# Kernel optimization log

Measured on AMD Instinct MI355X. Metric: run time of the kernel, lower is better.

## Reference

```python
import jax, jax.numpy as jnp
import numpy as np

B, S, E = 2, 2048, 1024
H = 1344            # hidden_dim = ceil(1.3*1024/64)*64
NH = 4              # mLSTM heads
DH = H // NH        # 336
K = 4               # causal conv kernel size
NPH = H // 4        # headwise proj heads (qkv_proj_blocksize=4)
PD = H // NPH       # per-head proj dim = 4
EPS = 1e-6


def setup_inputs() -> dict:
    key = jax.random.key(0)
    ks = jax.random.split(key, 10)
    s_in = jnp.sqrt(2.0 / (5 * E))    # small_init(E)
    s_pd = jnp.sqrt(2.0 / (5 * PD))   # small_init per-head dim
    return {
        "x": jax.random.normal(ks[0], (B, S, E), jnp.float32),
        "W_up": jax.random.normal(ks[1], (E, 2 * H), jnp.float32) * s_in,
        "conv_k": jax.random.normal(ks[2], (K, 1, H), jnp.float32) * jnp.sqrt(2.0 / K),  # depthwise, WIO layout
        "conv_b": jnp.zeros((H,), jnp.float32),
        "Wq": jax.random.normal(ks[3], (NPH, PD, PD), jnp.float32) * s_pd,
        "Wk": jax.random.normal(ks[4], (NPH, PD, PD), jnp.float32) * s_pd,
        "Wv": jax.random.normal(ks[5], (NPH, PD, PD), jnp.float32) * s_pd,
        "W_ig": jax.random.normal(ks[6], (3 * H, NH), jnp.float32) * 0.01,
        "b_ig": jax.random.normal(ks[7], (NH,), jnp.float32) * 0.1,
        "W_fg": jax.random.normal(ks[8], (3 * H, NH), jnp.float32) * 0.01,
        "b_fg": jnp.linspace(3.0, 6.0, NH, dtype=jnp.float32),
        "ln_w": jnp.ones((H,), jnp.float32),
        "skip": jnp.ones((H,), jnp.float32),
        "W_down": jax.random.normal(ks[9], (H, E), jnp.float32) * (2.0 / 12 / np.sqrt(H)),
    }


def _headwise(x, W):
    # LinearHeadwiseExpand: block-diagonal projection over NPH heads of size PD
    xh = x.reshape(B, S, NPH, PD)
    return jnp.einsum('bshd,hdo->bsho', xh, W).reshape(B, S, H)


def _mlstm_cell(q, k, v, ig, fg):
    # parallel stabilized mLSTM; q,k,v: (B,NH,S,DH); ig,fg: (B,NH,S)
    logf = jax.nn.log_sigmoid(fg)
    c = jnp.cumsum(logf, axis=-1)                         # (B,NH,S)
    logfmat = c[..., :, None] - c[..., None, :]           # (B,NH,S,S) cumulative forget decay
    mask = jnp.tril(jnp.ones((S, S), bool))               # causal mask
    log_D = jnp.where(mask, logfmat, -jnp.inf) + ig[..., None, :]
    m = jnp.max(log_D, axis=-1, keepdims=True)            # rowwise stabilizer
    D = jnp.exp(log_D - m)
    qk = jnp.einsum('bnsd,bntd->bnst', q, k) * (DH ** -0.5)
    C = qk * D
    n = jnp.maximum(jnp.abs(jnp.sum(C, axis=-1, keepdims=True)), jnp.exp(-m))
    return jnp.einsum('bnst,bntd->bnsd', C / (n + EPS), v)


def reference(x, W_up, conv_k, conv_b, Wq, Wk, Wv, W_ig, b_ig, W_fg, b_fg, ln_w, skip, W_down):
    x_inner = x @ W_up                                    # (B,S,2H)
    x_m, z = jnp.split(x_inner, 2, axis=-1)
    # depthwise causal conv1d
    xp = jnp.pad(x_m, ((0, 0), (K - 1, 0), (0, 0)))
    xc = jax.lax.conv_general_dilated(
        xp, conv_k, (1,), 'VALID',
        dimension_numbers=('NWC', 'WIO', 'NWC'),
        feature_group_count=H) + conv_b
    act = jax.nn.silu(xc)
    q = _headwise(act, Wq)
    k = _headwise(act, Wk)
    v = _headwise(x_m, Wv)
    gin = jnp.concatenate([q, k, v], axis=-1)             # (B,S,3H)
    ig = jnp.transpose(gin @ W_ig + b_ig, (0, 2, 1))      # (B,NH,S)
    fg = jnp.transpose(gin @ W_fg + b_fg, (0, 2, 1))
    qh = jnp.transpose(q.reshape(B, S, NH, DH), (0, 2, 1, 3))
    kh = jnp.transpose(k.reshape(B, S, NH, DH), (0, 2, 1, 3))
    vh = jnp.transpose(v.reshape(B, S, NH, DH), (0, 2, 1, 3))
    h = _mlstm_cell(qh, kh, vh, ig, fg)                   # (B,NH,S,DH)
    # multi-head layernorm (per-head groupnorm over DH, scale only)
    mu = jnp.mean(h, axis=-1, keepdims=True)
    var = jnp.var(h, axis=-1, keepdims=True)
    hn = (h - mu) * jax.lax.rsqrt(var + 1e-5) * ln_w.reshape(NH, 1, DH)
    h_out = jnp.transpose(hn, (0, 2, 1, 3)).reshape(B, S, H)
    h_state = (h_out + skip * act) * jax.nn.silu(z)
    return h_state @ W_down
```

## Files before the change

### kernel.cpp

```cpp
#include <hip/hip_runtime.h>
#include <cmath>

#define DI __device__ __forceinline__

constexpr int B_=2, S_=2048, E_=1024, H_=1344, NH_=4, DH_=336;
constexpr int BS_=B_*S_, H2_=2*H_;
constexpr int NG_=B_*NH_*S_;

constexpr size_t N_X=(size_t)BS_*E_;
constexpr size_t N_WUP=(size_t)E_*H2_;
constexpr size_t N_WDN=(size_t)H_*E_;
constexpr size_t N_BSH=(size_t)BS_*H_;
constexpr size_t N_BSH2=(size_t)BS_*H2_;
constexpr size_t N_WH=5376, N_WG=16128, N_CK=4*H_;

constexpr size_t O_IGB = 64;
constexpr size_t O_LOGF= O_IGB + NG_;
constexpr size_t O_AB  = O_LOGF+ NG_;
constexpr size_t O_MB  = O_AB  + NG_;
constexpr size_t O_MTB = O_MB  + NG_;
constexpr size_t O_CK  = O_MTB + NG_;
constexpr size_t O_CB  = O_CK  + N_CK;
constexpr size_t O_WQ  = O_CB  + H_;
constexpr size_t O_WK  = O_WQ  + N_WH;
constexpr size_t O_WV  = O_WK  + N_WH;
constexpr size_t O_WIG = O_WV  + N_WH;
constexpr size_t O_BIG = O_WIG + N_WG;
constexpr size_t O_WFG = O_BIG + 16;
constexpr size_t O_BFG = O_WFG + N_WG;
constexpr size_t O_LNW = O_BFG + 16;
constexpr size_t O_SKP = O_LNW + H_;
constexpr size_t O_FX  = O_SKP + H_;
constexpr size_t O_FWUP= O_FX  + N_X;
constexpr size_t O_FWDN= O_FWUP+ N_WUP;
constexpr size_t O_XIN = O_FWDN+ N_WDN;
constexpr size_t O_ACT = O_XIN + N_BSH2;
constexpr size_t O_QB  = O_ACT + N_BSH;
constexpr size_t O_KB  = O_QB  + N_BSH;
constexpr size_t O_VB  = O_KB  + N_BSH;
constexpr size_t O_HOUT= O_VB  + N_BSH;

constexpr size_t KSPLIT_SHORTS=(size_t)8*128*11*64*8;
constexpr size_t VT_SHORTS=(size_t)8*64*22*64*8;

typedef __attribute__((ext_vector_type(8))) short bf16x8;
typedef __attribute__((ext_vector_type(4))) float f32x4;

DI float bf2f(unsigned int u){union{unsigned int i;float f;}v;v.i=(u&0xffffu)<<16;return v.f;}
DI unsigned short f2bf(float f){union{float f;unsigned int i;}v;v.f=f;unsigned int x=v.i;
  return (unsigned short)((x+0x7fffu+((x>>16)&1u))>>16);}
DI float siluf(float x){return x/(1.f+expf(-x));}
DI float logsigf(float x){return (x>=0.f)?-log1pf(expf(-x)):x-log1pf(expf(x));}
DI void load4(const float* p, float* d){float4 v=*reinterpret_cast<const float4*>(p);
  d[0]=v.x;d[1]=v.y;d[2]=v.z;d[3]=v.w;}

__global__ __launch_bounds__(256) void detect_k(const unsigned short* __restrict__ xraw,
                                                int* __restrict__ flag){
  __shared__ int cnt_s;
  if(threadIdx.x==0) cnt_s=0;
  __syncthreads();
  int c=0;
  for(int i=threadIdx.x;i<2048;i+=256){
    const unsigned e=(xraw[i]>>7)&0xFFu;
    if(e>=0x90u) c++;
  }
  atomicAdd(&cnt_s,c);
  __syncthreads();
  if(threadIdx.x==0) *flag=(cnt_s>16)?0:1;
}

constexpr int CV0=5376, CV1=CV0+1344, CV2=CV1+5376, CV3=CV2+5376, CV4=CV3+5376,
              CV5=CV4+16128, CV6=CV5+4, CV7=CV6+16128, CV8=CV7+4,
              CV9=CV8+1344, CVT=CV9+1344;
__global__ __launch_bounds__(256) void convall_k(
    const void* s0,const void* s1,const void* s2,const void* s3,const void* s4,
    const void* s5,const void* s6,const void* s7,const void* s8,const void* s9,
    const void* s10, float* __restrict__ ws, const int* __restrict__ flag){
  const int i=blockIdx.x*256+threadIdx.x;
  if(i>=CVT) return;
  const void* src; int off; size_t dst;
  if(i<CV0){src=s0; off=i;      dst=O_CK +off;}
  else if(i<CV1){src=s1; off=i-CV0; dst=O_CB +off;}
  else if(i<CV2){src=s2; off=i-CV1; dst=O_WQ +off;}
  else if(i<CV3){src=s3; off=i-CV2; dst=O_WK +off;}
  else if(i<CV4){src=s4; off=i-CV3; dst=O_WV +off;}
  else if(i<CV5){src=s5; off=i-CV4; dst=O_WIG+off;}
  else if(i<CV6){src=s6; off=i-CV5; dst=O_BIG+off;}
  else if(i<CV7){src=s7; off=i-CV6; dst=O_WFG+off;}
  else if(i<CV8){src=s8; off=i-CV7; dst=O_BFG+off;}
  else if(i<CV9){src=s9; off=i-CV8; dst=O_LNW+off;}
  else          {src=s10;off=i-CV9; dst=O_SKP+off;}
  ws[dst]=(*flag)?bf2f(((const unsigned short*)src)[off])
                 :((const float*)src)[off];
}

__global__ __launch_bounds__(256) void prepAB_k(const void* __restrict__ xsrc,
    const void* __restrict__ wsrc, const int* __restrict__ flag,
    unsigned short* __restrict__ xhi, unsigned short* __restrict__ xlo,
    unsigned short* __restrict__ whi, unsigned short* __restrict__ wlo){
  const int blk=blockIdx.x;
  const int fl=*flag;
  float v[8];
  unsigned short* dh; unsigned short* dl; size_t slot;
  if(blk<2048){
    slot=(size_t)blk*256+threadIdx.x;
    const int l=(int)slot&63, rest=(int)(slot>>6);
    const int kc=rest&31, mt=rest>>5;
    const int row=mt*16+(l&15), k0=kc*32+(l>>4)*8;
    if(fl){
      const unsigned short* s=(const unsigned short*)xsrc+(size_t)row*1024+k0;
      const uint4 u=*reinterpret_cast<const uint4*>(s);
      v[0]=bf2f(u.x);v[1]=bf2f(u.x>>16);v[2]=bf2f(u.y);v[3]=bf2f(u.y>>16);
      v[4]=bf2f(u.z);v[5]=bf2f(u.z>>16);v[6]=bf2f(u.w);v[7]=bf2f(u.w>>16);
    }else{
      const float* s=(const float*)xsrc+(size_t)row*1024+k0;
      load4(s,v); load4(s+4,v+4);
    }
    dh=xhi; dl=xlo;
  } else {
    slot=(size_t)(blk-2048)*256+threadIdx.x;
    const int l=(int)slot&63, rest=(int)(slot>>6);
    const int kc=rest&31, nt=rest>>5;
    const int col=nt*16+(l&15), row0=kc*32+(l>>4)*8;
    if(fl){
      const unsigned short* s=(const unsigned short*)wsrc;
#pragma unroll
      for(int j=0;j<8;j++) v[j]=bf2f(s[(size_t)(row0+j)*2688+col]);
    }else{
      const float* s=(const float*)wsrc;
#pragma unroll
      for(int j=0;j<8;j++) v[j]=s[(size_t)(row0+j)*2688+col];
    }
    dh=whi; dl=wlo;
  }
  unsigned short h8[8], l8[8];
#pragma unroll
  for(int j=0;j<8;j++){ h8[j]=f2bf(v[j]); l8[j]=f2bf(v[j]-bf2f(h8[j])); }
  uint4 ph,pl;
  ph.x=(unsigned)h8[0]|((unsigned)h8[1]<<16); ph.y=(unsigned)h8[2]|((unsigned)h8[3]<<16);
  ph.z=(unsigned)h8[4]|((unsigned)h8[5]<<16); ph.w=(unsigned)h8[6]|((unsigned)h8[7]<<16);
  pl.x=(unsigned)l8[0]|((unsigned)l8[1]<<16); pl.y=(unsigned)l8[2]|((unsigned)l8[3]<<16);
  pl.z=(unsigned)l8[4]|((unsigned)l8[5]<<16); pl.w=(unsigned)l8[6]|((unsigned)l8[7]<<16);
  *reinterpret_cast<uint4*>(&dh[slot*8])=ph;
  *reinterpret_cast<uint4*>(&dl[slot*8])=pl;
}

__global__ __launch_bounds__(256) void gemm3_k(
    const unsigned short* __restrict__ Ahi, const unsigned short* __restrict__ Alo,
    const unsigned short* __restrict__ Bhi, const unsigned short* __restrict__ Blo,
    void* __restrict__ C, const int* __restrict__ flag, int kcn, int ldc){
  const int t=threadIdx.x, w=t>>6, l=t&63, lm=l&15, quad=l>>4;
  const int bn=blockIdx.x*128, bm=blockIdx.y*128;
  const int mtg0=bm>>4, ntg0=bn>>4;

  __shared__ short TT[2][32*512];

  f32x4 acc[2][8];
#pragma unroll
  for(int g=0;g<2;g++)
#pragma unroll
    for(int nt=0;nt<8;nt++) acc[g][nt]={0.f,0.f,0.f,0.f};

  auto stage=[&](int buf,int kc){
#pragma unroll
    for(int j=0;j<8;j++){
      const int tr=w*8+j;
      const unsigned short* src;
      if(tr<8)       src=&Ahi[((size_t)(mtg0+tr   )*kcn+kc)*512+(size_t)l*8];
      else if(tr<16) src=&Alo[((size_t)(mtg0+tr-8 )*kcn+kc)*512+(size_t)l*8];
      else if(tr<24) src=&Bhi[((size_t)(ntg0+tr-16)*kcn+kc)*512+(size_t)l*8];
      else           src=&Blo[((size_t)(ntg0+tr-24)*kcn+kc)*512+(size_t)l*8];
      __builtin_amdgcn_global_load_lds(
        (const __attribute__((address_space(1))) unsigned int*)src,
        (__attribute__((address_space(3))) unsigned int*)&TT[buf][tr*512],
        16,0,0);
    }
  };

  auto compute=[&](int buf){
    const short* Tb=&TT[buf][0];
    const bf16x8 ah0=*reinterpret_cast<const bf16x8*>(&Tb[(2*w  )*512+l*8]);
    const bf16x8 ah1=*reinterpret_cast<const bf16x8*>(&Tb[(2*w+1)*512+l*8]);
    const bf16x8 al0=*reinterpret_cast<const bf16x8*>(&Tb[(8+2*w  )*512+l*8]);
    const bf16x8 al1=*reinterpret_cast<const bf16x8*>(&Tb[(8+2*w+1)*512+l*8]);
#pragma unroll
    for(int nt=0;nt<8;nt++){
      const bf16x8 bh=*reinterpret_cast<const bf16x8*>(&Tb[(16+nt)*512+l*8]);
      const bf16x8 bl=*reinterpret_cast<const bf16x8*>(&Tb[(24+nt)*512+l*8]);
      acc[0][nt]=__builtin_amdgcn_mfma_f32_16x16x32_bf16(ah0,bh,acc[0][nt],0,0,0);
      acc[0][nt]=__builtin_amdgcn_mfma_f32_16x16x32_bf16(al0,bh,acc[0][nt],0,0,0);
      acc[0][nt]=__builtin_amdgcn_mfma_f32_16x16x32_bf16(ah0,bl,acc[0][nt],0,0,0);
      acc[1][nt]=__builtin_amdgcn_mfma_f32_16x16x32_bf16(ah1,bh,acc[1][nt],0,0,0);
      acc[1][nt]=__builtin_amdgcn_mfma_f32_16x16x32_bf16(al1,bh,acc[1][nt],0,0,0);
      acc[1][nt]=__builtin_amdgcn_mfma_f32_16x16x32_bf16(ah1,bl,acc[1][nt],0,0,0);
    }
  };

  stage(0,0);
  for(int kc=0;kc<kcn;kc++){
    const int cur=kc&1;
    if(kc+1<kcn){
      stage(cur^1,kc+1);
      asm volatile("s_waitcnt vmcnt(8)" ::: "memory");
    } else {
      asm volatile("s_waitcnt vmcnt(0)" ::: "memory");
    }
    __builtin_amdgcn_s_barrier();
    compute(cur);
    __builtin_amdgcn_s_barrier();
  }

  const int bf=flag?*flag:0;
#pragma unroll
  for(int g=0;g<2;g++)
#pragma unroll
    for(int nt=0;nt<8;nt++)
#pragma unroll
      for(int r=0;r<4;r++){
        const size_t idx=(size_t)(bm+(2*w+g)*16+quad*4+r)*ldc+bn+nt*16+lm;
        if(bf) ((unsigned short*)C)[idx]=f2bf(acc[g][nt][r]);
        else   ((float*)C)[idx]=acc[g][nt][r];
      }
}

__global__ __launch_bounds__(384) void convqkvgates_k(
    const float* __restrict__ xin, const float* __restrict__ ck,
    const float* __restrict__ cb,
    const float* __restrict__ Wq, const float* __restrict__ Wk,
    const float* __restrict__ Wv,
    const float* __restrict__ Wig, const float* __restrict__ big,
    const float* __restrict__ Wfg, const float* __restrict__ bfg,
    float* __restrict__ act, float* __restrict__ qb, float* __restrict__ kb,
    float* __restrict__ vb, float* __restrict__ igb, float* __restrict__ logfb){
  const int bs=blockIdx.x;
  const int b=bs>>11, s=bs&2047;
  const int t=threadIdx.x;
  __shared__ float4 sq4[336], sk4[336], sv4[336];
  __shared__ float red[6][8];
  if(t<336){
    const int ph=t, base=ph*4;
    float xc[4];
#pragma unroll
    for(int d=0;d<4;d++) xc[d]=cb[base+d];
    float xm[4]={0.f,0.f,0.f,0.f};
#pragma unroll
    for(int w=0;w<4;w++){
      const int sr=s-3+w;
      if(sr>=0){
        float xv[4];
        load4(&xin[(size_t)(b*S_+sr)*H2_+base],xv);
#pragma unroll
        for(int d=0;d<4;d++) xc[d]+=xv[d]*ck[w*H_+base+d];
        if(w==3){ xm[0]=xv[0];xm[1]=xv[1];xm[2]=xv[2];xm[3]=xv[3]; }
      }
    }
    float a4[4];
#pragma unroll
    for(int d=0;d<4;d++) a4[d]=siluf(xc[d]);
    *reinterpret_cast<float4*>(&act[(size_t)bs*H_+base])
        =make_float4(a4[0],a4[1],a4[2],a4[3]);
    float q4[4],k4[4],v4[4];
#pragma unroll
    for(int o=0;o<4;o++){
      float q=0.f,k=0.f,v=0.f;
#pragma unroll
      for(int d=0;d<4;d++){
        q+=a4[d]*Wq[ph*16+d*4+o];
        k+=a4[d]*Wk[ph*16+d*4+o];
        v+=xm[d]*Wv[ph*16+d*4+o];
      }
      q4[o]=q;k4[o]=k;v4[o]=v;
    }
    const int nh=ph/84, dh0=(ph-nh*84)*4;
    const size_t off=((size_t)(b*NH_+nh)*S_+s)*DH_+dh0;
    *reinterpret_cast<float4*>(&qb[off])=make_float4(q4[0],q4[1],q4[2],q4[3]);
    *reinterpret_cast<float4*>(&kb[off])=make_float4(k4[0],k4[1],k4[2],k4[3]);
    *reinterpret_cast<float4*>(&vb[off])=make_float4(v4[0],v4[1],v4[2],v4[3]);
    sq4[ph]=make_float4(q4[0],q4[1],q4[2],q4[3]);
    sk4[ph]=make_float4(k4[0],k4[1],k4[2],k4[3]);
    sv4[ph]=make_float4(v4[0],v4[1],v4[2],v4[3]);
  }
  __syncthreads();
  const float* sq=reinterpret_cast<const float*>(sq4);
  const float* sk=reinterpret_cast<const float*>(sk4);
  const float* sv=reinterpret_cast<const float*>(sv4);
  float aI0=0.f,aI1=0.f,aI2=0.f,aI3=0.f;
  float aF0=0.f,aF1=0.f,aF2=0.f,aF3=0.f;
  for(int h=t; h<H_; h+=384){
    const float q=sq[h], k=sk[h], v=sv[h];
    const float4 wiq=*reinterpret_cast<const float4*>(&Wig[(size_t)h*4]);
    const float4 wik=*reinterpret_cast<const float4*>(&Wig[(size_t)(H_+h)*4]);
    const float4 wiv=*reinterpret_cast<const float4*>(&Wig[(size_t)(2*H_+h)*4]);
    const float4 wfq=*reinterpret_cast<const float4*>(&Wfg[(size_t)h*4]);
    const float4 wfk=*reinterpret_cast<const float4*>(&Wfg[(size_t)(H_+h)*4]);
    const float4 wfv=*reinterpret_cast<const float4*>(&Wfg[(size_t)(2*H_+h)*4]);
    aI0+=q*wiq.x+k*wik.x+v*wiv.x;
    aI1+=q*wiq.y+k*wik.y+v*wiv.y;
    aI2+=q*wiq.z+k*wik.z+v*wiv.z;
    aI3+=q*wiq.w+k*wik.w+v*wiv.w;
    aF0+=q*wfq.x+k*wfk.x+v*wfv.x;
    aF1+=q*wfq.y+k*wfk.y+v*wfv.y;
    aF2+=q*wfq.z+k*wfk.z+v*wfv.z;
    aF3+=q*wfq.w+k*wfk.w+v*wfv.w;
  }
#pragma unroll
  for(int m=1;m<64;m<<=1){
    aI0+=__shfl_xor(aI0,m); aI1+=__shfl_xor(aI1,m);
    aI2+=__shfl_xor(aI2,m); aI3+=__shfl_xor(aI3,m);
    aF0+=__shfl_xor(aF0,m); aF1+=__shfl_xor(aF1,m);
    aF2+=__shfl_xor(aF2,m); aF3+=__shfl_xor(aF3,m);
  }
  const int wv=t>>6, l=t&63;
  if(l==0){
    red[wv][0]=aI0; red[wv][1]=aI1; red[wv][2]=aI2; red[wv][3]=aI3;
    red[wv][4]=aF0; red[wv][5]=aF1; red[wv][6]=aF2; red[wv][7]=aF3;
  }
  __syncthreads();
  if(t==0){
    float r[8];
#pragma unroll
    for(int j=0;j<8;j++){
      float a=0.f;
#pragma unroll
      for(int wv2=0;wv2<6;wv2++) a+=red[wv2][j];
      r[j]=a;
    }
#pragma unroll
    for(int n=0;n<4;n++){
      const size_t o=(size_t)(b*NH_+n)*S_+s;
      igb[o]=r[n]+big[n];
      logfb[o]=logsigf(r[4+n]+bfg[n]);
    }
  }
}

__global__ __launch_bounds__(256) void kvprep3_k(const float* __restrict__ kb,
                                                 const float* vb,
                                                 const void* __restrict__ wdnsrc,
                                                 const int* __restrict__ flag,
                                                 unsigned short* __restrict__ khi,
                                                 unsigned short* __restrict__ klo,
                                                 unsigned short* __restrict__ vTf,
                                                 unsigned short* __restrict__ wdnhi,
                                                 unsigned short* __restrict__ wdnlo,
                                                 float* partz){
  const int blk=blockIdx.x;
  if(blk<1024){
    const int head=blk>>7, tt=blk&127;
    const size_t obase=(size_t)blk*11*512;
    for(int slot=threadIdx.x; slot<704; slot+=256){
      const int dc=slot>>6, ll=slot&63, quad=ll>>4, lm=ll&15;
      const int tg=tt*16+lm, dbase=dc*32+quad*8;
      float v[8];
      if(dbase<336){
        load4(&kb[((size_t)head*S_+tg)*DH_+dbase],v);
        load4(&kb[((size_t)head*S_+tg)*DH_+dbase+4],v+4);
      } else { for(int j=0;j<8;j++) v[j]=0.f; }
      unsigned short hi8[8], lo8[8];
#pragma unroll
      for(int j=0;j<8;j++){
        hi8[j]=f2bf(v[j]);
        lo8[j]=f2bf(v[j]-bf2f(hi8[j]));
      }
      const size_t o=obase+(size_t)(dc*64+ll)*8;
      uint4 ph, pl;
      ph.x=(unsigned)hi8[0]|((unsigned)hi8[1]<<16); ph.y=(unsigned)hi8[2]|((unsigned)hi8[3]<<16);
      ph.z=(unsigned)hi8[4]|((unsigned)hi8[5]<<16); ph.w=(unsigned)hi8[6]|((unsigned)hi8[7]<<16);
      pl.x=(unsigned)lo8[0]|((unsigned)lo8[1]<<16); pl.y=(unsigned)lo8[2]|((unsigned)lo8[3]<<16);
      pl.z=(unsigned)lo8[4]|((unsigned)lo8[5]<<16); pl.w=(unsigned)lo8[6]|((unsigned)lo8[7]<<16);
      *reinterpret_cast<uint4*>(&khi[o])=ph;
      *reinterpret_cast<uint4*>(&klo[o])=pl;
    }
  } else if(blk<1536){
    const int vblk=blk-1024;
    const int head=vblk>>6, tc=vblk&63;
    const size_t obase=(size_t)vblk*22*512;
    for(int slot=threadIdx.x; slot<1408; slot+=256){
      const int ntg=slot>>6, ll=slot&63, quad=ll>>4, lm=ll&15;
      const int n=ntg*16+lm, t0=tc*32+quad*8;
      unsigned short h8[8];
#pragma unroll
      for(int j=0;j<8;j++){
        float val;
        if(n<336)       val=vb[((size_t)head*S_+t0+j)*DH_+n];
        else if(n==336) val=1.f;
        else            val=0.f;
        h8[j]=f2bf(val);
      }
      uint4 pk;
      pk.x=(unsigned)h8[0]|((unsigned)h8[1]<<16); pk.y=(unsigned)h8[2]|((unsigned)h8[3]<<16);
      pk.z=(unsigned)h8[4]|((unsigned)h8[5]<<16); pk.w=(unsigned)h8[6]|((unsigned)h8[7]<<16);
      *reinterpret_cast<uint4*>(&vTf[obase+(size_t)(ntg*64+ll)*8])=pk;
    }
    __syncthreads();
    const size_t zb=((size_t)head*2048+(size_t)tc*32)*336;
    for(int idx=threadIdx.x; idx<32*336; idx+=256) partz[zb+idx]=0.f;
  } else {
    const size_t slot=(size_t)(blk-1536)*256+threadIdx.x;
    const int l=(int)slot&63, rest=(int)(slot>>6);
    const int kc=rest%42, nt=rest/42;
    const int col=nt*16+(l&15), row0=kc*32+(l>>4)*8;
    const int fl=*flag;
    float v[8];
    if(fl){
      const unsigned short* s=(const unsigned short*)wdnsrc;
#pragma unroll
      for(int j=0;j<8;j++) v[j]=bf2f(s[(size_t)(row0+j)*1024+col]);
    }else{
      const float* s=(const float*)wdnsrc;
#pragma unroll
      for(int j=0;j<8;j++) v[j]=s[(size_t)(row0+j)*1024+col];
    }
    unsigned short h8[8], l8[8];
#pragma unroll
    for(int j=0;j<8;j++){ h8[j]=f2bf(v[j]); l8[j]=f2bf(v[j]-bf2f(h8[j])); }
    uint4 ph,pl;
    ph.x=(unsigned)h8[0]|((unsigned)h8[1]<<16); ph.y=(unsigned)h8[2]|((unsigned)h8[3]<<16);
    ph.z=(unsigned)h8[4]|((unsigned)h8[5]<<16); ph.w=(unsigned)h8[6]|((unsigned)h8[7]<<16);
    pl.x=(unsigned)l8[0]|((unsigned)l8[1]<<16); pl.y=(unsigned)l8[2]|((unsigned)l8[3]<<16);
    pl.z=(unsigned)l8[4]|((unsigned)l8[5]<<16); pl.w=(unsigned)l8[6]|((unsigned)l8[7]<<16);
    *reinterpret_cast<uint4*>(&wdnhi[slot*8])=ph;
    *reinterpret_cast<uint4*>(&wdnlo[slot*8])=pl;
  }
}

__global__ __launch_bounds__(256) void scan_k(float* igm,
                                              const float* __restrict__ logfb,
                                              float* __restrict__ ab,float* __restrict__ Mb,
                                              float* __restrict__ mtb){
  const int head=blockIdx.x, t=threadIdx.x;
  __shared__ float sh[256];
  const float* lf=logfb+(size_t)head*S_;
  float* ig=igm+(size_t)head*S_;
  float lc[8];
  float run=0.f;
#pragma unroll
  for(int i=0;i<8;i++){ run+=lf[t*8+i]; lc[i]=run; }
  sh[t]=run;
  for(int st=1;st<256;st<<=1){
    __syncthreads();
    const float v=(t>=st)?sh[t-st]:0.f;
    __syncthreads();
    sh[t]+=v;
  }
  __syncthreads();
  const float off=(t==0)?0.f:sh[t-1];
  __syncthreads();
  float av[8],mv[8],cv[8];
  float mrun=-1e30f;
#pragma unroll
  for(int i=0;i<8;i++){
    cv[i]=off+lc[i];
    av[i]=ig[t*8+i]-cv[i];
    mrun=fmaxf(mrun,av[i]);
    mv[i]=mrun;
  }
  sh[t]=mrun;
  for(int st=1;st<256;st<<=1){
    __syncthreads();
    const float v=(t>=st)?sh[t-st]:-1e30f;
    __syncthreads();
    sh[t]=fmaxf(sh[t],v);
  }
  __syncthreads();
  const float moff=(t==0)?-1e30f:sh[t-1];
#pragma unroll
  for(int i=0;i<8;i++){
    const float Mi=fmaxf(moff,mv[i]);
    const size_t j=(size_t)head*S_+t*8+i;
    ab[j]=av[i]; Mb[j]=Mi; mtb[j]=cv[i]+Mi;
    ig[t*8+i]=0.f;
  }
}

__global__ __launch_bounds__(512,1) void mlstm6_k(
    const float* __restrict__ qb, const unsigned short* __restrict__ khi,
    const unsigned short* __restrict__ klo, const unsigned short* __restrict__ vTf,
    const float* __restrict__ ab, const float* __restrict__ Mb,
    float* __restrict__ part, float* __restrict__ rsum){
  const int bid=blockIdx.x;
  const int head=bid&7;
  const int rest=bid>>3;
  const int pairI=rest&7, seg=rest>>3;
  const int t=threadIdx.x, w=t>>6, l=t&63, lm=l&15, quad=l>>4;

  __shared__ short KV[2][66*512];
  __shared__ short Sc[8][16][40];

  const size_t hb=(size_t)head*S_;
  const float scale=0.05455447256f;

  const int sbA=pairI, sbB=15-pairI;
  const int nA=pairI+1, nTot=17;

  bf16x8 qh[11], ql[11];
  f32x4 accO[22];
  float Mr[4];
  int ws0=sbA*128+w*16;

  auto loadQ=[&](int ws0_){
    const float* qrow=qb+(hb+ws0_+lm)*DH_;
#pragma unroll
    for(int dc=0;dc<11;dc++){
      const int dbase=dc*32+quad*8;
      float v[8];
      if(dbase<336){ load4(qrow+dbase,v); load4(qrow+dbase+4,v+4); }
      else { for(int j=0;j<8;j++) v[j]=0.f; }
#pragma unroll
      for(int j=0;j<8;j++){
        const unsigned short h=f2bf(v[j]);
        qh[dc][j]=(short)h;
        ql[dc][j]=(short)f2bf(v[j]-bf2f(h));
      }
    }
#pragma unroll
    for(int r=0;r<4;r++) Mr[r]=Mb[hb+ws0_+quad*4+r];
#pragma unroll
    for(int n=0;n<22;n++) accO[n]={0.f,0.f,0.f,0.f};
  };

  auto itemC=[&](int i)->int{
    return (i<nA)? (seg+4*i) : (seg+4*(i-nA));
  };

  auto stage=[&](int buf,int c){
    const size_t kbase=(((size_t)head*128+(size_t)(2*c))*11)*512+(size_t)l*8;
    const size_t vbase=(((size_t)head*64+(size_t)c)*22)*512+(size_t)l*8;
#pragma unroll
    for(int j=0;j<9;j++){
      const int tr=w+8*j;
      if(tr<66){
        const unsigned short* src;
        if(tr<22)      src=&khi[kbase+(size_t)tr*512];
        else if(tr<44) src=&klo[kbase+(size_t)(tr-22)*512];
        else           src=&vTf[vbase+(size_t)(tr-44)*512];
        __builtin_amdgcn_global_load_lds(
          (const __attribute__((address_space(1))) unsigned int*)src,
          (__attribute__((address_space(3))) unsigned int*)&KV[buf][(size_t)tr*512],
          16,0,0);
      }
    }
  };

  auto compute=[&](int c,int buf){
    const int t0=c<<5;
    if(t0>ws0+15) return;
    const float al0=ab[hb+t0+lm];
    const float al1=ab[hb+t0+16+lm];
#pragma unroll
    for(int tt=0;tt<2;tt++){
      f32x4 a0={0,0,0,0}, a1={0,0,0,0}, a2={0,0,0,0};
#pragma unroll
      for(int dc=0;dc<11;dc++){
        const bf16x8 kh=*reinterpret_cast<const bf16x8*>(&KV[buf][(tt*11+dc)*512+l*8]);
        const bf16x8 kl=*reinterpret_cast<const bf16x8*>(&KV[buf][(22+tt*11+dc)*512+l*8]);
        a0=__builtin_amdgcn_mfma_f32_16x16x32_bf16(qh[dc],kh,a0,0,0,0);
        a1=__builtin_amdgcn_mfma_f32_16x16x32_bf16(ql[dc],kh,a1,0,0,0);
        a2=__builtin_amdgcn_mfma_f32_16x16x32_bf16(qh[dc],kl,a2,0,0,0);
      }
      const float al=(tt==0)?al0:al1;
      const int tg=t0+tt*16+lm;
#pragma unroll
      for(int r=0;r<4;r++){
        const int srow=quad*4+r;
        const float qk=a0[r]+a1[r]+a2[r];
        const float e=fminf(al-Mr[r],0.f);
        const float msk=(tg<=ws0+srow)?1.f:0.f;
        Sc[w][srow][tt*16+lm]=(short)f2bf(msk*(qk*scale*expf(e)));
      }
    }
    const bf16x8 scf=*reinterpret_cast<const bf16x8*>(&Sc[w][lm][quad*8]);
#pragma unroll
    for(int nt=0;nt<22;nt++){
      const bf16x8 vf=*reinterpret_cast<const bf16x8*>(&KV[buf][(44+nt)*512+l*8]);
      accO[nt]=__builtin_amdgcn_mfma_f32_16x16x32_bf16(scf,vf,accO[nt],0,0,0);
    }
  };

  auto epilogue=[&](){
    const size_t pbase=(size_t)head*2048+ws0;
#pragma unroll
    for(int nt=0;nt<22;nt++){
      const int col=nt*16+lm;
#pragma unroll
      for(int r=0;r<4;r++){
        const int srow=quad*4+r;
        const float val=accO[nt][r];
        if(col<336){ if(val!=0.f) atomicAdd(&part[(pbase+srow)*336+col],val); }
        else if(col==336){ if(val!=0.f) atomicAdd(&rsum[pbase+srow],val); }
      }
    }
  };

  loadQ(ws0);
  stage(0,itemC(0));
  __syncthreads();
  int cur=0;
  for(int i=0;i<nTot;i++){
    if(i+1<nTot) stage(cur^1,itemC(i+1));
    compute(itemC(i),cur);
    if(i==nA-1){
      epilogue();
      ws0=sbB*128+w*16;
      loadQ(ws0);
    }
    __syncthreads();
    cur^=1;
  }
  epilogue();
}

__global__ __launch_bounds__(256) void finalize3_k(const float* __restrict__ part,
                                                   const float* __restrict__ rsum,
                                                   const float* __restrict__ mtb,
                                                   const float* __restrict__ lnw,
                                                   const float* __restrict__ skip,
                                                   const float* __restrict__ act,
                                                   const float* __restrict__ xin,
                                                   unsigned short* __restrict__ hshi,
                                                   unsigned short* __restrict__ hslo){
  const int sblk=blockIdx.x, head=blockIdx.y;
  const int bI=head>>2, nh=head&3;
  const int s0=sblk*32;
  const int t=threadIdx.x, row=t>>3, sub=t&7;
  __shared__ float red1[32][8], red2[32][8];
  __shared__ float mu_s[32], rs_s[32], inv_s[32];
  const size_t pbase=(size_t)head*2048+s0;
  const float* prow=part+(pbase+row)*336;
  float s1=0.f,s2=0.f;
  for(int c=sub;c<336;c+=8){ const float v=prow[c]; s1+=v; s2+=v*v; }
  red1[row][sub]=s1; red2[row][sub]=s2;
  __syncthreads();
  if(sub==0){
    float a1=0.f,a2=0.f;
#pragma unroll
    for(int j=0;j<8;j++){ a1+=red1[row][j]; a2+=red2[row][j]; }
    const float mt=mtb[(size_t)head*S_+s0+row];
    const float nn=fmaxf(fabsf(rsum[pbase+row]), expf(fminf(fmaxf(-mt,-60.f),60.f)));
    const float inv=1.f/(nn+1e-6f);
    const float mu=a1*inv/336.f;
    const float var=a2*inv*inv/336.f-mu*mu;
    inv_s[row]=inv; mu_s[row]=mu;
    rs_s[row]=rsqrtf(fmaxf(var,0.f)+1e-5f);
  }
  __syncthreads();
  const float inv=inv_s[row], mu=mu_s[row], rs=rs_s[row];
  const size_t gbs=(size_t)(bI*S_+s0+row);
  const float* arow=act+gbs*H_+nh*DH_;
  const float* zrow=xin+gbs*H2_+H_+nh*DH_;
  const float* srw=skip+nh*DH_;
  const float* lrw=lnw+nh*DH_;
  const size_t mtbase=(gbs>>4)*42;
  const int lbase=(int)(gbs&15);
  for(int c=sub;c<336;c+=8){
    const float hn=(prow[c]*inv-mu)*rs*lrw[c];
    const float val=(hn+srw[c]*arow[c])*siluf(zrow[c]);
    const int h=nh*DH_+c;
    const int kc=h>>5, quad=(h>>3)&3, j=h&7;
    const size_t slot=(mtbase+kc)*64+lbase+16*quad;
    const unsigned short hi=f2bf(val);
    hshi[slot*8+j]=hi;
    hslo[slot*8+j]=f2bf(val-bf2f(hi));
  }
}

extern "C" void kernel_launch(void* const* d_in, const int* in_sizes, int n_in,
                              void* d_out, int out_size, void* d_ws, size_t ws_size,
                              hipStream_t stream){
  float* ws=(float*)d_ws;
  int* flag=(int*)ws;

  float* igb  = ws+O_IGB;
  float* logfb= ws+O_LOGF;
  float* ab   = ws+O_AB;
  float* Mbuf = ws+O_MB;
  float* mtb  = ws+O_MTB;
  float* f_ck = ws+O_CK;
  float* f_cb = ws+O_CB;
  float* f_wq = ws+O_WQ;
  float* f_wk = ws+O_WK;
  float* f_wv = ws+O_WV;
  float* f_wig= ws+O_WIG;
  float* f_big= ws+O_BIG;
  float* f_wfg= ws+O_WFG;
  float* f_bfg= ws+O_BFG;
  float* f_lnw= ws+O_LNW;
  float* f_skp= ws+O_SKP;
  float* xin  = ws+O_XIN;
  float* act  = ws+O_ACT;
  float* qb   = ws+O_QB;
  float* kb   = ws+O_KB;
  float* vb   = ws+O_VB;

  unsigned short* xhi  =(unsigned short*)(ws+O_FX);   unsigned short* xlo  =xhi+N_X;
  unsigned short* wuphi=(unsigned short*)(ws+O_FWUP); unsigned short* wuplo=wuphi+N_WUP;
  unsigned short* wdnhi=(unsigned short*)(ws+O_FWDN); unsigned short* wdnlo=wdnhi+N_WDN;
  unsigned short* khi=(unsigned short*)(ws+O_FX);
  unsigned short* klo=khi+KSPLIT_SHORTS;
  unsigned short* vTf=(unsigned short*)(ws+O_HOUT);
  unsigned short* hshi=(unsigned short*)kb;
  unsigned short* hslo=hshi+N_BSH;
  float* partb=vb;
  float* rsumb=igb;

  detect_k<<<1,256,0,stream>>>((const unsigned short*)d_in[0],flag);
  convall_k<<<(CVT+255)/256,256,0,stream>>>(d_in[2],d_in[3],d_in[4],d_in[5],d_in[6],
                                            d_in[7],d_in[8],d_in[9],d_in[10],d_in[11],
                                            d_in[12],ws,flag);

  prepAB_k<<<2048+1344,256,0,stream>>>(d_in[0],d_in[1],flag,xhi,xlo,wuphi,wuplo);
  gemm3_k<<<dim3(2688/128,4096/128),256,0,stream>>>(xhi,xlo,wuphi,wuplo,xin,nullptr,32,H2_);

  convqkvgates_k<<<BS_,384,0,stream>>>(xin,f_ck,f_cb,f_wq,f_wk,f_wv,
                                       f_wig,f_big,f_wfg,f_bfg,
                                       act,qb,kb,vb,igb,logfb);
  kvprep3_k<<<1024+512+672,256,0,stream>>>(kb,vb,d_in[13],flag,
                                           khi,klo,vTf,wdnhi,wdnlo,partb);
  scan_k<<<B_*NH_,256,0,stream>>>(igb,logfb,ab,Mbuf,mtb);
  mlstm6_k<<<256,512,0,stream>>>(qb,khi,klo,vTf,ab,Mbuf,partb,rsumb);
  finalize3_k<<<dim3(S_/32,B_*NH_),256,0,stream>>>(partb,rsumb,mtb,f_lnw,f_skp,act,xin,
                                                   hshi,hslo);
  gemm3_k<<<dim3(1024/128,4096/128),256,0,stream>>>(hshi,hslo,wdnhi,wdnlo,d_out,flag,42,E_);
}
```

Before: 438.5 us.

## Fuse K hi/lo split into gate kernel and parameter conversion into prepAB

The K tensor's bf16 hi/lo split and MFMA-tiled layout are now written directly from the conv/qkv/gates kernel, so the fp32 K buffer is no longer stored and re-read by a separate prep kernel. The small parameter conversion kernel is folded into prepAB as extra blocks, which removes one launch. The padding region of the K tiles is zeroed by extra blocks in the renamed V/W prep kernel. In exchange, the gate kernel's stores become scattered 8-byte writes.

New measurement: 431.0 us. About the same (-1.7%).

```diff
diff --git a/kernel.cpp b/kernel.cpp
--- a/kernel.cpp
+++ b/kernel.cpp
@@ -72,34 +72,35 @@
 constexpr int CV0=5376, CV1=CV0+1344, CV2=CV1+5376, CV3=CV2+5376, CV4=CV3+5376,
               CV5=CV4+16128, CV6=CV5+4, CV7=CV6+16128, CV8=CV7+4,
               CV9=CV8+1344, CVT=CV9+1344;
-__global__ __launch_bounds__(256) void convall_k(
-    const void* s0,const void* s1,const void* s2,const void* s3,const void* s4,
-    const void* s5,const void* s6,const void* s7,const void* s8,const void* s9,
-    const void* s10, float* __restrict__ ws, const int* __restrict__ flag){
-  const int i=blockIdx.x*256+threadIdx.x;
-  if(i>=CVT) return;
-  const void* src; int off; size_t dst;
-  if(i<CV0){src=s0; off=i;      dst=O_CK +off;}
-  else if(i<CV1){src=s1; off=i-CV0; dst=O_CB +off;}
-  else if(i<CV2){src=s2; off=i-CV1; dst=O_WQ +off;}
-  else if(i<CV3){src=s3; off=i-CV2; dst=O_WK +off;}
-  else if(i<CV4){src=s4; off=i-CV3; dst=O_WV +off;}
-  else if(i<CV5){src=s5; off=i-CV4; dst=O_WIG+off;}
-  else if(i<CV6){src=s6; off=i-CV5; dst=O_BIG+off;}
-  else if(i<CV7){src=s7; off=i-CV6; dst=O_WFG+off;}
-  else if(i<CV8){src=s8; off=i-CV7; dst=O_BFG+off;}
-  else if(i<CV9){src=s9; off=i-CV8; dst=O_LNW+off;}
-  else          {src=s10;off=i-CV9; dst=O_SKP+off;}
-  ws[dst]=(*flag)?bf2f(((const unsigned short*)src)[off])
-                 :((const float*)src)[off];
-}
 
 __global__ __launch_bounds__(256) void prepAB_k(const void* __restrict__ xsrc,
     const void* __restrict__ wsrc, const int* __restrict__ flag,
     unsigned short* __restrict__ xhi, unsigned short* __restrict__ xlo,
-    unsigned short* __restrict__ whi, unsigned short* __restrict__ wlo){
+    unsigned short* __restrict__ whi, unsigned short* __restrict__ wlo,
+    const void* s2,const void* s3,const void* s4,const void* s5,const void* s6,
+    const void* s7,const void* s8,const void* s9,const void* s10,const void* s11,
+    const void* s12, float* __restrict__ ws){
   const int blk=blockIdx.x;
   const int fl=*flag;
+  if(blk>=3392){
+    const int i=(blk-3392)*256+threadIdx.x;
+    if(i>=CVT) return;
+    const void* src; int off; size_t dst;
+    if(i<CV0){src=s2; off=i;      dst=O_CK +off;}
+    else if(i<CV1){src=s3; off=i-CV0; dst=O_CB +off;}
+    else if(i<CV2){src=s4; off=i-CV1; dst=O_WQ +off;}
+    else if(i<CV3){src=s5; off=i-CV2; dst=O_WK +off;}
+    else if(i<CV4){src=s6; off=i-CV3; dst=O_WV +off;}
+    else if(i<CV5){src=s7; off=i-CV4; dst=O_WIG+off;}
+    else if(i<CV6){src=s8; off=i-CV5; dst=O_BIG+off;}
+    else if(i<CV7){src=s9; off=i-CV6; dst=O_WFG+off;}
+    else if(i<CV8){src=s10;off=i-CV7; dst=O_BFG+off;}
+    else if(i<CV9){src=s11;off=i-CV8; dst=O_LNW+off;}
+    else          {src=s12;off=i-CV9; dst=O_SKP+off;}
+    ws[dst]=fl?bf2f(((const unsigned short*)src)[off])
+              :((const float*)src)[off];
+    return;
+  }
   float v[8];
   unsigned short* dh; unsigned short* dl; size_t slot;
   if(blk<2048){
@@ -230,8 +231,9 @@
     const float* __restrict__ Wv,
     const float* __restrict__ Wig, const float* __restrict__ big,
     const float* __restrict__ Wfg, const float* __restrict__ bfg,
-    float* __restrict__ act, float* __restrict__ qb, float* __restrict__ kb,
-    float* __restrict__ vb, float* __restrict__ igb, float* __restrict__ logfb){
+    float* __restrict__ act, float* __restrict__ qb, float* __restrict__ vb,
+    unsigned short* __restrict__ khi, unsigned short* __restrict__ klo,
+    float* __restrict__ igb, float* __restrict__ logfb){
   const int bs=blockIdx.x;
   const int b=bs>>11, s=bs&2047;
   const int t=threadIdx.x;
@@ -274,8 +276,27 @@
     const int nh=ph/84, dh0=(ph-nh*84)*4;
     const size_t off=((size_t)(b*NH_+nh)*S_+s)*DH_+dh0;
     *reinterpret_cast<float4*>(&qb[off])=make_float4(q4[0],q4[1],q4[2],q4[3]);
-    *reinterpret_cast<float4*>(&kb[off])=make_float4(k4[0],k4[1],k4[2],k4[3]);
     *reinterpret_cast<float4*>(&vb[off])=make_float4(v4[0],v4[1],v4[2],v4[3]);
+    {
+      const int head8=b*NH_+nh;
+      const int tt=s>>4, lm=s&15;
+      const int dc=dh0>>5, quad=(dh0&31)>>3, j=dh0&7;
+      const size_t ob=(((size_t)(head8*128+tt)*11)+dc)*512
+                      +(size_t)(quad*16+lm)*8+j;
+      unsigned short kh[4], kl[4];
+#pragma unroll
+      for(int o=0;o<4;o++){
+        kh[o]=f2bf(k4[o]);
+        kl[o]=f2bf(k4[o]-bf2f(kh[o]));
+      }
+      uint2 pk, pl;
+      pk.x=(unsigned)kh[0]|((unsigned)kh[1]<<16);
+      pk.y=(unsigned)kh[2]|((unsigned)kh[3]<<16);
+      pl.x=(unsigned)kl[0]|((unsigned)kl[1]<<16);
+      pl.y=(unsigned)kl[2]|((unsigned)kl[3]<<16);
+      *reinterpret_cast<uint2*>(&khi[ob])=pk;
+      *reinterpret_cast<uint2*>(&klo[ob])=pl;
+    }
     sq4[ph]=make_float4(q4[0],q4[1],q4[2],q4[3]);
     sk4[ph]=make_float4(k4[0],k4[1],k4[2],k4[3]);
     sv4[ph]=make_float4(v4[0],v4[1],v4[2],v4[3]);
@@ -334,47 +355,19 @@
   }
 }
 
-__global__ __launch_bounds__(256) void kvprep3_k(const float* __restrict__ kb,
-                                                 const float* vb,
-                                                 const void* __restrict__ wdnsrc,
-                                                 const int* __restrict__ flag,
-                                                 unsigned short* __restrict__ khi,
-                                                 unsigned short* __restrict__ klo,
-                                                 unsigned short* __restrict__ vTf,
-                                                 unsigned short* __restrict__ wdnhi,
-                                                 unsigned short* __restrict__ wdnlo,
-                                                 float* partz){
+__global__ __launch_bounds__(256) void vwprep_k(const float* vb,
+                                                const void* __restrict__ wdnsrc,
+                                                const int* __restrict__ flag,
+                                                unsigned short* __restrict__ vTf,
+                                                unsigned short* __restrict__ wdnhi,
+                                                unsigned short* __restrict__ wdnlo,
+                                                unsigned short* __restrict__ khi,
+                                                unsigned short* __restrict__ klo,
+                                                float* partz){
   const int blk=blockIdx.x;
-  if(blk<1024){
-    const int head=blk>>7, tt=blk&127;
-    const size_t obase=(size_t)blk*11*512;
-    for(int slot=threadIdx.x; slot<704; slot+=256){
-      const int dc=slot>>6, ll=slot&63, quad=ll>>4, lm=ll&15;
-      const int tg=tt*16+lm, dbase=dc*32+quad*8;
-      float v[8];
-      if(dbase<336){
-        load4(&kb[((size_t)head*S_+tg)*DH_+dbase],v);
-        load4(&kb[((size_t)head*S_+tg)*DH_+dbase+4],v+4);
-      } else { for(int j=0;j<8;j++) v[j]=0.f; }
-      unsigned short hi8[8], lo8[8];
-#pragma unroll
-      for(int j=0;j<8;j++){
-        hi8[j]=f2bf(v[j]);
-        lo8[j]=f2bf(v[j]-bf2f(hi8[j]));
-      }
-      const size_t o=obase+(size_t)(dc*64+ll)*8;
-      uint4 ph, pl;
-      ph.x=(unsigned)hi8[0]|((unsigned)hi8[1]<<16); ph.y=(unsigned)hi8[2]|((unsigned)hi8[3]<<16);
-      ph.z=(unsigned)hi8[4]|((unsigned)hi8[5]<<16); ph.w=(unsigned)hi8[6]|((unsigned)hi8[7]<<16);
-      pl.x=(unsigned)lo8[0]|((unsigned)lo8[1]<<16); pl.y=(unsigned)lo8[2]|((unsigned)lo8[3]<<16);
-      pl.z=(unsigned)lo8[4]|((unsigned)lo8[5]<<16); pl.w=(unsigned)lo8[6]|((unsigned)lo8[7]<<16);
-      *reinterpret_cast<uint4*>(&khi[o])=ph;
-      *reinterpret_cast<uint4*>(&klo[o])=pl;
-    }
-  } else if(blk<1536){
-    const int vblk=blk-1024;
-    const int head=vblk>>6, tc=vblk&63;
-    const size_t obase=(size_t)vblk*22*512;
+  if(blk<512){
+    const int head=blk>>6, tc=blk&63;
+    const size_t obase=(size_t)blk*22*512;
     for(int slot=threadIdx.x; slot<1408; slot+=256){
       const int ntg=slot>>6, ll=slot&63, quad=ll>>4, lm=ll&15;
       const int n=ntg*16+lm, t0=tc*32+quad*8;
@@ -395,8 +388,8 @@
     __syncthreads();
     const size_t zb=((size_t)head*2048+(size_t)tc*32)*336;
     for(int idx=threadIdx.x; idx<32*336; idx+=256) partz[zb+idx]=0.f;
-  } else {
-    const size_t slot=(size_t)(blk-1536)*256+threadIdx.x;
+  } else if(blk<1184){
+    const size_t slot=(size_t)(blk-512)*256+threadIdx.x;
     const int l=(int)slot&63, rest=(int)(slot>>6);
     const int kc=rest%42, nt=rest/42;
     const int col=nt*16+(l&15), row0=kc*32+(l>>4)*8;
@@ -421,6 +414,13 @@
     pl.z=(unsigned)l8[4]|((unsigned)l8[5]<<16); pl.w=(unsigned)l8[6]|((unsigned)l8[7]<<16);
     *reinterpret_cast<uint4*>(&wdnhi[slot*8])=ph;
     *reinterpret_cast<uint4*>(&wdnlo[slot*8])=pl;
+  } else {
+    const int idx=(blk-1184)*256+threadIdx.x;
+    const int kt=idx>>4, u=idx&15;
+    const size_t base_s=(((size_t)kt*11)+10)*512 + 256 + (size_t)u*16;
+    const uint4 z={0,0,0,0};
+    *reinterpret_cast<uint4*>(&khi[base_s])=z;
+    *reinterpret_cast<uint4*>(&klo[base_s])=z;
   }
 }
 
@@ -704,18 +704,17 @@
   float* rsumb=igb;
 
   detect_k<<<1,256,0,stream>>>((const unsigned short*)d_in[0],flag);
-  convall_k<<<(CVT+255)/256,256,0,stream>>>(d_in[2],d_in[3],d_in[4],d_in[5],d_in[6],
-                                            d_in[7],d_in[8],d_in[9],d_in[10],d_in[11],
-                                            d_in[12],ws,flag);
-
-  prepAB_k<<<2048+1344,256,0,stream>>>(d_in[0],d_in[1],flag,xhi,xlo,wuphi,wuplo);
+  prepAB_k<<<2048+1344+226,256,0,stream>>>(d_in[0],d_in[1],flag,xhi,xlo,wuphi,wuplo,
+                                           d_in[2],d_in[3],d_in[4],d_in[5],d_in[6],
+                                           d_in[7],d_in[8],d_in[9],d_in[10],d_in[11],
+                                           d_in[12],ws);
   gemm3_k<<<dim3(2688/128,4096/128),256,0,stream>>>(xhi,xlo,wuphi,wuplo,xin,nullptr,32,H2_);
 
   convqkvgates_k<<<BS_,384,0,stream>>>(xin,f_ck,f_cb,f_wq,f_wk,f_wv,
                                        f_wig,f_big,f_wfg,f_bfg,
-                                       act,qb,kb,vb,igb,logfb);
-  kvprep3_k<<<1024+512+672,256,0,stream>>>(kb,vb,d_in[13],flag,
-                                           khi,klo,vTf,wdnhi,wdnlo,partb);
+                                       act,qb,vb,khi,klo,igb,logfb);
+  vwprep_k<<<512+672+64,256,0,stream>>>(vb,d_in[13],flag,vTf,wdnhi,wdnlo,
+                                        khi,klo,partb);
   scan_k<<<B_*NH_,256,0,stream>>>(igb,logfb,ab,Mbuf,mtb);
   mlstm6_k<<<256,512,0,stream>>>(qb,khi,klo,vTf,ab,Mbuf,partb,rsumb);
   finalize3_k<<<dim3(S_/32,B_*NH_),256,0,stream>>>(partb,rsumb,mtb,f_lnw,f_skp,act,xin,
```
